# Performance work log

Measured on AMD Instinct MI355X. Metric: run time of the kernel, lower is better.

The kernel has to match this reference:

```python
import jax, jax.numpy as jnp
import numpy as np

N = 50000
E = 800000
IN_F = 128
HID = 128
OUT_F = 64
MU = 2.0
EPS = 1e-12


def setup_inputs() -> dict:
    key = jax.random.key(0)
    ks = jax.random.split(key, 20)
    d = {}
    d["x"] = jax.random.normal(ks[0], (N, IN_F), dtype=jnp.float32)
    d["edge_src"] = jax.random.randint(ks[1], (E,), 0, N, dtype=jnp.int32)
    d["edge_dst"] = jax.random.randint(ks[2], (E,), 0, N, dtype=jnp.int32)
    d["edge_val"] = jax.random.uniform(ks[3], (E,), dtype=jnp.float32)
    # layer 0: in=128 -> pool=128 -> out=128 (activation=relu)
    s0 = 1.0 / np.sqrt(IN_F)
    d["pool_w0"] = jax.random.uniform(ks[4], (IN_F, IN_F), jnp.float32, -s0, s0)
    d["pool_b0"] = jax.random.uniform(ks[5], (IN_F,), jnp.float32, -s0, s0)
    d["fc1_w0"] = jax.random.uniform(ks[6], (HID, IN_F), jnp.float32, -s0, s0)
    d["fc1_b0"] = jax.random.uniform(ks[7], (HID,), jnp.float32, -s0, s0)
    d["fc2_w0"] = jax.random.uniform(ks[8], (HID, IN_F), jnp.float32, -s0, s0)
    d["fc2_b0"] = jax.random.uniform(ks[9], (HID,), jnp.float32, -s0, s0)
    # layer 1 (final): in=128 -> pool=128 -> out=64 (no activation)
    s1 = 1.0 / np.sqrt(HID)
    d["pool_w1"] = jax.random.uniform(ks[10], (HID, HID), jnp.float32, -s1, s1)
    d["pool_b1"] = jax.random.uniform(ks[11], (HID,), jnp.float32, -s1, s1)
    d["fc1_w1"] = jax.random.uniform(ks[12], (OUT_F, HID), jnp.float32, -s1, s1)
    d["fc1_b1"] = jax.random.uniform(ks[13], (OUT_F,), jnp.float32, -s1, s1)
    d["fc2_w1"] = jax.random.uniform(ks[14], (OUT_F, HID), jnp.float32, -s1, s1)
    d["fc2_b1"] = jax.random.uniform(ks[15], (OUT_F,), jnp.float32, -s1, s1)
    return d


def _sage_conv(x, src, dst, val, pw, pb, w1, b1, w2, b2, act):
    # L2-normalize rows (F.normalize(x, dim=1))
    xn = x / jnp.maximum(jnp.linalg.norm(x, axis=1, keepdims=True), EPS)
    h = jax.nn.relu(xn @ pw.T + pb)               # [N, pool]
    h_mu = h ** MU                                # elementwise pow
    # spmm(adj, h_mu): gather source rows, scale by edge weight, scatter-add to dst rows
    agg = jax.ops.segment_sum(h_mu[src] * val[:, None], dst, num_segments=N)
    agg = agg ** (1.0 / MU)                       # generalized-mean root
    out = (h @ w1.T + b1) + (agg @ w2.T + b2)
    return jax.nn.relu(out) if act else out


def reference(x, edge_src, edge_dst, edge_val,
              pool_w0, pool_b0, fc1_w0, fc1_b0, fc2_w0, fc2_b0,
              pool_w1, pool_b1, fc1_w1, fc1_b1, fc2_w1, fc2_b1):
    h = _sage_conv(x, edge_src, edge_dst, edge_val,
                   pool_w0, pool_b0, fc1_w0, fc1_b0, fc2_w0, fc2_b0, act=True)
    out = _sage_conv(h, edge_src, edge_dst, edge_val,
                     pool_w1, pool_b1, fc1_w1, fc1_b1, fc2_w1, fc2_b1, act=False)
    return out
```

## Files before the change

### kernel.cpp

```cpp
#include <hip/hip_runtime.h>

#define FF 128
#define BCAP 8192
#define CHUNK 4096
#define PITCH 136
#define BSTRIDE 32
#define PBCACHE 6144

typedef __attribute__((ext_vector_type(8))) short short8;
typedef __attribute__((ext_vector_type(4))) float f32x4;
typedef __attribute__((ext_vector_type(4))) int i32x4;
typedef __attribute__((ext_vector_type(2))) int i32x2;

__device__ __forceinline__ unsigned short bf16_rne(float f) {
    unsigned u = __float_as_uint(f);
    u += 0x7fffu + ((u >> 16) & 1u);
    return (unsigned short)(u >> 16);
}
__device__ __forceinline__ float bf16_to_f32(unsigned short h) {
    return __uint_as_float(((unsigned)h) << 16);
}

__global__ __launch_bounds__(256, 2)
void poolpartA_kernel(const float* __restrict__ x,
                      const unsigned short* __restrict__ Wh, const unsigned short* __restrict__ Wl,
                      const float* __restrict__ bias,
                      unsigned short* __restrict__ hout,
                      const int* __restrict__ esrc, const int* __restrict__ edst,
                      const float* __restrict__ eval,
                      int* __restrict__ bucket_cnt, int2* __restrict__ ebuf,
                      int N, int E, int nchunks)
{
    __shared__ alignas(16) char smem[37888];
    const int t = threadIdx.x;

    if (blockIdx.x < nchunks) {
        int* cnt   = (int*)smem;
        int* sc    = cnt + 256;
        int* excl  = sc + 256;
        int* cur   = excl + 256;
        int* gbase = cur + 256;
        int2* staged = (int2*)(smem + 5 * 256 * 4);
        const int e0 = blockIdx.x * CHUNK;
        const int n  = min(CHUNK, E - e0);

        unsigned pk[16]; float vr[16];
        #pragma unroll
        for (int k = 0; k < 16; ++k) {
            const int i = t + k * 256;
            pk[k] = 0xFFFFFFFFu;
            if (i < n) {
                int d = edst[e0 + i];
                int s = esrc[e0 + i];
                pk[k] = (unsigned)((s & 0xffff) | (d << 16));
                vr[k] = eval[e0 + i];
            }
        }

        cnt[t] = 0;
        __syncthreads();
        #pragma unroll
        for (int k = 0; k < 16; ++k)
            if (pk[k] != 0xFFFFFFFFu) atomicAdd(&cnt[pk[k] >> 24], 1);
        __syncthreads();

        sc[t] = cnt[t];
        __syncthreads();
        #pragma unroll
        for (int off = 1; off < 256; off <<= 1) {
            int v = (t >= off) ? sc[t - off] : 0;
            __syncthreads();
            sc[t] += v;
            __syncthreads();
        }
        excl[t] = sc[t] - cnt[t];
        cur[t]  = excl[t];
        if (cnt[t] > 0) gbase[t] = atomicAdd(&bucket_cnt[t * BSTRIDE], cnt[t]);
        __syncthreads();

        #pragma unroll
        for (int k = 0; k < 16; ++k) {
            if (pk[k] != 0xFFFFFFFFu) {
                int b = pk[k] >> 24;
                int slot = atomicAdd(&cur[b], 1);
                staged[slot] = make_int2((int)pk[k], __float_as_int(vr[k]));
            }
        }
        __syncthreads();

        for (int p = t; p < n; p += 256) {
            int2 ent = staged[p];
            int b = ((unsigned)ent.x) >> 24;
            int gpos = gbase[b] + (p - excl[b]);
            ebuf[(size_t)b * BCAP + gpos] = ent;
        }
    } else {
        unsigned short* sX = (unsigned short*)smem;
        float* sNorm = (float*)(smem + 64 * PITCH * 2);
        const int tile = blockIdx.x - nchunks;

        #pragma unroll
        for (int rg = 0; rg < 2; ++rg) {
            const int row = rg * 32 + (t >> 3);
            const int c0  = (t & 7) * 16;
            const int n   = tile * 64 + row;
            const int base = row * PITCH + c0;
            float v[16];
            if (n < N) {
                const float4* p = (const float4*)(x + (size_t)n * FF + c0);
                #pragma unroll
                for (int i = 0; i < 4; ++i) {
                    float4 q = p[i];
                    v[4*i] = q.x; v[4*i+1] = q.y; v[4*i+2] = q.z; v[4*i+3] = q.w;
                }
            } else {
                #pragma unroll
                for (int i = 0; i < 16; ++i) v[i] = 0.f;
            }
            float ss = 0.f;
            #pragma unroll
            for (int i = 0; i < 16; ++i) ss = fmaf(v[i], v[i], ss);
            union { unsigned short u[8]; short8 s; } h0, h1;
            #pragma unroll
            for (int i = 0; i < 8; ++i) {
                h0.u[i] = bf16_rne(v[i]);
                h1.u[i] = bf16_rne(v[8 + i]);
            }
            *(short8*)&sX[base]     = h0.s;
            *(short8*)&sX[base + 8] = h1.s;
            ss += __shfl_xor(ss, 1);
            ss += __shfl_xor(ss, 2);
            ss += __shfl_xor(ss, 4);
            if ((t & 7) == 0) sNorm[row] = 1.0f / fmaxf(sqrtf(ss), 1e-12f);
        }
        __syncthreads();

        const int lane = t & 63, wave = t >> 6;
        const int quad = lane >> 4, l16 = lane & 15;

        short8 Bh[2][4], Bl[2][4];
        #pragma unroll
        for (int c = 0; c < 2; ++c) {
            const int jt = 2 * wave + c;
            #pragma unroll
            for (int tt = 0; tt < 4; ++tt) {
                const size_t o = ((size_t)(jt * 4 + tt) * 64 + lane) * 8;
                Bh[c][tt] = *(const short8*)&Wh[o];
                Bl[c][tt] = *(const short8*)&Wl[o];
            }
        }

        f32x4 acc[4][2];
        #pragma unroll
        for (int r = 0; r < 4; ++r)
            #pragma unroll
            for (int c = 0; c < 2; ++c) {
                f32x4 z = {0.f, 0.f, 0.f, 0.f};
                acc[r][c] = z;
            }

        #pragma unroll
        for (int tt = 0; tt < 4; ++tt) {
            short8 Ah[4];
            #pragma unroll
            for (int r = 0; r < 4; ++r)
                Ah[r] = *(const short8*)&sX[(r * 16 + l16) * PITCH + tt * 32 + quad * 8];
            #pragma unroll
            for (int c = 0; c < 2; ++c)
                #pragma unroll
                for (int r = 0; r < 4; ++r) {
                    acc[r][c] = __builtin_amdgcn_mfma_f32_16x16x32_bf16(Ah[r], Bh[c][tt], acc[r][c], 0, 0, 0);
                    acc[r][c] = __builtin_amdgcn_mfma_f32_16x16x32_bf16(Ah[r], Bl[c][tt], acc[r][c], 0, 0, 0);
                }
        }

        __syncthreads();
        #pragma unroll
        for (int c = 0; c < 2; ++c) {
            const int j = (2 * wave + c) * 16 + l16;
            const float bj = bias[j];
            #pragma unroll
            for (int r = 0; r < 4; ++r) {
                #pragma unroll
                for (int g = 0; g < 4; ++g) {
                    const int nl = r * 16 + quad * 4 + g;
                    float s = sNorm[nl];
                    float val = fmaf(acc[r][c][g], s, bj);
                    val = fmaxf(val, 0.f);
                    sX[nl * PITCH + j] = bf16_rne(val);
                }
            }
        }
        __syncthreads();
        #pragma unroll
        for (int rg = 0; rg < 2; ++rg) {
            const int row = rg * 32 + (t >> 3);
            const int c0  = (t & 7) * 16;
            const int n   = tile * 64 + row;
            if (n < N) {
                const int base = row * PITCH + c0;
                *(short8*)&hout[(size_t)n * FF + c0]     = *(short8*)&sX[base];
                *(short8*)&hout[(size_t)n * FF + c0 + 8] = *(short8*)&sX[base + 8];
            }
        }
    }
}

struct WPack {
    const float* src[6];
    unsigned short* hi[6];
    unsigned short* lo[6];
    int n[6];
};

__global__ __launch_bounds__(256)
void wprep_kernel(WPack p, int* __restrict__ bucket_cnt)
{
    if (blockIdx.x == 0) {
        for (int i = threadIdx.x; i < 256 * BSTRIDE; i += 256) bucket_cnt[i] = 0;
    }
    int id = blockIdx.x * 256 + threadIdx.x;
    #pragma unroll
    for (int i = 0; i < 6; ++i) {
        if (id < p.n[i]) {
            float f = p.src[i][id];
            unsigned short h = bf16_rne(f);
            const int j = id >> 7, k = id & 127;
            const int jt = j >> 4, l16 = j & 15;
            const int t = k >> 5, quad = (k >> 3) & 3, j8 = k & 7;
            const size_t o = ((size_t)((jt * 4 + t) * 4 + quad) * 16 + l16) * 8 + j8;
            p.hi[i][o] = h;
            p.lo[i][o] = bf16_rne(f - bf16_to_f32(h));
            return;
        }
        id -= p.n[i];
    }
}

__global__ __launch_bounds__(256)
void partB_kernel(const int* __restrict__ bucket_cnt, const int2* __restrict__ ebuf,
                  int* __restrict__ offsets, int2* __restrict__ edata,
                  int N, int E, int nbuck)
{
    __shared__ int pre[256], hist[256], sc[256], excl[256], cur[256];
    __shared__ int2 sBuf[PBCACHE];
    const int t = threadIdx.x;
    const int b = blockIdx.x;

    const int cnt_self = bucket_cnt[b * BSTRIDE];
    const int2* ib = ebuf + (size_t)b * BCAP;
    const bool useL = (cnt_self <= PBCACHE);

    if (useL)
        for (int i = t; i < cnt_self; i += 256) sBuf[i] = ib[i];

    pre[t] = (t < nbuck) ? bucket_cnt[t * BSTRIDE] : 0;
    hist[t] = 0;
    __syncthreads();
    #pragma unroll
    for (int off = 1; off < 256; off <<= 1) {
        int v = (t >= off) ? pre[t - off] : 0;
        __syncthreads();
        pre[t] += v;
        __syncthreads();
    }
    const int base = (b == 0) ? 0 : pre[b - 1];
    const int cnt  = cnt_self;

    for (int i = t; i < cnt; i += 256) {
        int2 ent = useL ? sBuf[i] : ib[i];
        atomicAdd(&hist[(((unsigned)ent.x) >> 16) & 255], 1);
    }
    __syncthreads();

    sc[t] = hist[t];
    __syncthreads();
    #pragma unroll
    for (int off = 1; off < 256; off <<= 1) {
        int v = (t >= off) ? sc[t - off] : 0;
        __syncthreads();
        sc[t] += v;
        __syncthreads();
    }
    excl[t] = sc[t] - hist[t];
    cur[t]  = excl[t];

    const int node = b * 256 + t;
    if (node <= N) offsets[node] = base + excl[t];
    __syncthreads();

    for (int i = t; i < cnt; i += 256) {
        int2 ent = useL ? sBuf[i] : ib[i];
        int l = (((unsigned)ent.x) >> 16) & 255;
        int pos = base + atomicAdd(&cur[l], 1);
        edata[pos] = make_int2(ent.x & 0xffff, ent.y);
    }
}

__device__ __forceinline__ void fma4sq(float4& a, float v, uint2 u) {
    float f0 = __uint_as_float(u.x << 16);
    float f1 = __uint_as_float(u.x & 0xffff0000u);
    float f2 = __uint_as_float(u.y << 16);
    float f3 = __uint_as_float(u.y & 0xffff0000u);
    a.x = fmaf(v * f0, f0, a.x);
    a.y = fmaf(v * f1, f1, a.y);
    a.z = fmaf(v * f2, f2, a.z);
    a.w = fmaf(v * f3, f3, a.w);
}

__device__ __forceinline__ i32x4 ldnt4(const int2* p) {
    return __builtin_nontemporal_load((const i32x4*)p);
}
__device__ __forceinline__ i32x2 ldnt2(const int2* p) {
    return __builtin_nontemporal_load((const i32x2*)p);
}

__global__ __launch_bounds__(256)
void agg_kernel(const unsigned short* __restrict__ hp, const int* __restrict__ offsets,
                const int2* __restrict__ edata,
                unsigned short* __restrict__ aggh, int N)
{
    const int w = blockIdx.x * 8 + (threadIdx.x >> 5);
    if (w >= N) return;
    const int l = threadIdx.x & 31;
    const size_t fo = (size_t)(l * 4);
    int e = offsets[w];
    const int end = offsets[w + 1];

    float4 a0 = {0,0,0,0}, a1 = {0,0,0,0}, a2 = {0,0,0,0}, a3 = {0,0,0,0};

    if ((e & 1) && e < end) {
        i32x2 ed = ldnt2(&edata[e]);
        uint2 u = *(const uint2*)&hp[(size_t)ed[0] * FF + fo];
        fma4sq(a0, __int_as_float(ed[1]), u);
        ++e;
    }
    for (; e + 7 < end; e += 8) {
        i32x4 p0 = ldnt4(&edata[e]);
        i32x4 p1 = ldnt4(&edata[e + 2]);
        i32x4 p2 = ldnt4(&edata[e + 4]);
        i32x4 p3 = ldnt4(&edata[e + 6]);
        uint2 u0 = *(const uint2*)&hp[(size_t)p0[0] * FF + fo];
        uint2 u1 = *(const uint2*)&hp[(size_t)p0[2] * FF + fo];
        uint2 u2 = *(const uint2*)&hp[(size_t)p1[0] * FF + fo];
        uint2 u3 = *(const uint2*)&hp[(size_t)p1[2] * FF + fo];
        uint2 u4 = *(const uint2*)&hp[(size_t)p2[0] * FF + fo];
        uint2 u5 = *(const uint2*)&hp[(size_t)p2[2] * FF + fo];
        uint2 u6 = *(const uint2*)&hp[(size_t)p3[0] * FF + fo];
        uint2 u7 = *(const uint2*)&hp[(size_t)p3[2] * FF + fo];
        fma4sq(a0, __int_as_float(p0[1]), u0);
        fma4sq(a1, __int_as_float(p0[3]), u1);
        fma4sq(a2, __int_as_float(p1[1]), u2);
        fma4sq(a3, __int_as_float(p1[3]), u3);
        fma4sq(a0, __int_as_float(p2[1]), u4);
        fma4sq(a1, __int_as_float(p2[3]), u5);
        fma4sq(a2, __int_as_float(p3[1]), u6);
        fma4sq(a3, __int_as_float(p3[3]), u7);
    }
    if (e + 3 < end) {
        i32x4 p0 = ldnt4(&edata[e]);
        i32x4 p1 = ldnt4(&edata[e + 2]);
        uint2 u0 = *(const uint2*)&hp[(size_t)p0[0] * FF + fo];
        uint2 u1 = *(const uint2*)&hp[(size_t)p0[2] * FF + fo];
        uint2 u2 = *(const uint2*)&hp[(size_t)p1[0] * FF + fo];
        uint2 u3 = *(const uint2*)&hp[(size_t)p1[2] * FF + fo];
        fma4sq(a0, __int_as_float(p0[1]), u0);
        fma4sq(a1, __int_as_float(p0[3]), u1);
        fma4sq(a2, __int_as_float(p1[1]), u2);
        fma4sq(a3, __int_as_float(p1[3]), u3);
        e += 4;
    }
    if (e + 1 < end) {
        i32x4 p = ldnt4(&edata[e]);
        uint2 u0 = *(const uint2*)&hp[(size_t)p[0] * FF + fo];
        uint2 u1 = *(const uint2*)&hp[(size_t)p[2] * FF + fo];
        fma4sq(a0, __int_as_float(p[1]), u0);
        fma4sq(a1, __int_as_float(p[3]), u1);
        e += 2;
    }
    if (e < end) {
        i32x2 ed = ldnt2(&edata[e]);
        uint2 u = *(const uint2*)&hp[(size_t)ed[0] * FF + fo];
        fma4sq(a0, __int_as_float(ed[1]), u);
    }

    float4 r;
    r.x = sqrtf(a0.x + a1.x + a2.x + a3.x);
    r.y = sqrtf(a0.y + a1.y + a2.y + a3.y);
    r.z = sqrtf(a0.z + a1.z + a2.z + a3.z);
    r.w = sqrtf(a0.w + a1.w + a2.w + a3.w);

    uint2 hv = { (unsigned)bf16_rne(r.x) | ((unsigned)bf16_rne(r.y) << 16),
                 (unsigned)bf16_rne(r.z) | ((unsigned)bf16_rne(r.w) << 16) };
    *(uint2*)&aggh[(size_t)w * FF + fo] = hv;
}

__global__ __launch_bounds__(256, 2)
void mm2pool_kernel(const unsigned short* __restrict__ hin,
                    const unsigned short* __restrict__ aggh,
                    const unsigned short* __restrict__ W1h, const unsigned short* __restrict__ W1l,
                    const unsigned short* __restrict__ W2h, const unsigned short* __restrict__ W2l,
                    const float* __restrict__ b1, const float* __restrict__ b2,
                    const unsigned short* __restrict__ PWh, const unsigned short* __restrict__ PWl,
                    const float* __restrict__ pb,
                    unsigned short* __restrict__ hout, int N)
{
    __shared__ unsigned short sH[64 * PITCH];
    __shared__ unsigned short sA[64 * PITCH];
    __shared__ float sNorm[64];

    const int tid  = threadIdx.x;
    const int tile = blockIdx.x;

    #pragma unroll
    for (int rg = 0; rg < 2; ++rg) {
        const int row = rg * 32 + (tid >> 3);
        const int c0  = (tid & 7) * 16;
        const int n   = tile * 64 + row;
        const int base = row * PITCH + c0;
        short8 z = {0,0,0,0,0,0,0,0};
        short8 a = z, b = z, c = z, d = z;
        if (n < N) {
            const short8* ph = (const short8*)(hin  + (size_t)n * FF + c0);
            const short8* pa = (const short8*)(aggh + (size_t)n * FF + c0);
            a = ph[0]; b = ph[1];
            c = pa[0]; d = pa[1];
        }
        *(short8*)&sH[base]     = a;
        *(short8*)&sH[base + 8] = b;
        *(short8*)&sA[base]     = c;
        *(short8*)&sA[base + 8] = d;
    }
    __syncthreads();

    const int lane = tid & 63, wave = tid >> 6;
    const int quad = lane >> 4, l16 = lane & 15;

    short8 B1hf[2][4], B1lf[2][4], B2hf[2][4], B2lf[2][4];
    #pragma unroll
    for (int c = 0; c < 2; ++c) {
        const int jt = 2 * wave + c;
        #pragma unroll
        for (int t = 0; t < 4; ++t) {
            const size_t o = ((size_t)(jt * 4 + t) * 64 + lane) * 8;
            B1hf[c][t] = *(const short8*)&W1h[o];
            B1lf[c][t] = *(const short8*)&W1l[o];
            B2hf[c][t] = *(const short8*)&W2h[o];
            B2lf[c][t] = *(const short8*)&W2l[o];
        }
    }

    f32x4 acc[4][2];
    #pragma unroll
    for (int r = 0; r < 4; ++r)
        #pragma unroll
        for (int c = 0; c < 2; ++c) {
            f32x4 z = {0.f, 0.f, 0.f, 0.f};
            acc[r][c] = z;
        }

    #pragma unroll
    for (int t = 0; t < 4; ++t) {
        short8 Hf[4], AH[4];
        #pragma unroll
        for (int r = 0; r < 4; ++r) {
            const int off = (r * 16 + l16) * PITCH + t * 32 + quad * 8;
            Hf[r] = *(const short8*)&sH[off];
            AH[r] = *(const short8*)&sA[off];
        }
        #pragma unroll
        for (int c = 0; c < 2; ++c)
            #pragma unroll
            for (int r = 0; r < 4; ++r) {
                acc[r][c] = __builtin_amdgcn_mfma_f32_16x16x32_bf16(Hf[r], B1hf[c][t], acc[r][c], 0, 0, 0);
                acc[r][c] = __builtin_amdgcn_mfma_f32_16x16x32_bf16(Hf[r], B1lf[c][t], acc[r][c], 0, 0, 0);
                acc[r][c] = __builtin_amdgcn_mfma_f32_16x16x32_bf16(AH[r], B2hf[c][t], acc[r][c], 0, 0, 0);
                acc[r][c] = __builtin_amdgcn_mfma_f32_16x16x32_bf16(AH[r], B2lf[c][t], acc[r][c], 0, 0, 0);
            }
    }

    __syncthreads();

    #pragma unroll
    for (int c = 0; c < 2; ++c) {
        const int j = (2 * wave + c) * 16 + l16;
        const float bj = b1[j] + b2[j];
        #pragma unroll
        for (int r = 0; r < 4; ++r) {
            #pragma unroll
            for (int g = 0; g < 4; ++g) {
                const int nl = r * 16 + quad * 4 + g;
                float val = fmaxf(acc[r][c][g] + bj, 0.f);
                sH[nl * PITCH + j] = bf16_rne(val);
            }
        }
    }
    __syncthreads();

    #pragma unroll
    for (int rg = 0; rg < 2; ++rg) {
        const int row = rg * 32 + (tid >> 3);
        const int c0  = (tid & 7) * 16;
        union { short8 s; unsigned short u[8]; } a, b;
        a.s = *(short8*)&sH[row * PITCH + c0];
        b.s = *(short8*)&sH[row * PITCH + c0 + 8];
        float ss = 0.f;
        #pragma unroll
        for (int i = 0; i < 8; ++i) {
            float fa = bf16_to_f32(a.u[i]);
            float fb = bf16_to_f32(b.u[i]);
            ss = fmaf(fa, fa, fmaf(fb, fb, ss));
        }
        ss += __shfl_xor(ss, 1);
        ss += __shfl_xor(ss, 2);
        ss += __shfl_xor(ss, 4);
        if ((tid & 7) == 0) sNorm[row] = 1.0f / fmaxf(sqrtf(ss), 1e-12f);
    }
    __syncthreads();

    short8 Ph[2][4], Pl[2][4];
    #pragma unroll
    for (int c = 0; c < 2; ++c) {
        const int jt = 2 * wave + c;
        #pragma unroll
        for (int t = 0; t < 4; ++t) {
            const size_t o = ((size_t)(jt * 4 + t) * 64 + lane) * 8;
            Ph[c][t] = *(const short8*)&PWh[o];
            Pl[c][t] = *(const short8*)&PWl[o];
        }
    }

    f32x4 acc2[4][2];
    #pragma unroll
    for (int r = 0; r < 4; ++r)
        #pragma unroll
        for (int c = 0; c < 2; ++c) {
            f32x4 z = {0.f, 0.f, 0.f, 0.f};
            acc2[r][c] = z;
        }

    #pragma unroll
    for (int t = 0; t < 4; ++t) {
        short8 Ah[4];
        #pragma unroll
        for (int r = 0; r < 4; ++r)
            Ah[r] = *(const short8*)&sH[(r * 16 + l16) * PITCH + t * 32 + quad * 8];
        #pragma unroll
        for (int c = 0; c < 2; ++c)
            #pragma unroll
            for (int r = 0; r < 4; ++r) {
                acc2[r][c] = __builtin_amdgcn_mfma_f32_16x16x32_bf16(Ah[r], Ph[c][t], acc2[r][c], 0, 0, 0);
                acc2[r][c] = __builtin_amdgcn_mfma_f32_16x16x32_bf16(Ah[r], Pl[c][t], acc2[r][c], 0, 0, 0);
            }
    }

    __syncthreads();
    #pragma unroll
    for (int c = 0; c < 2; ++c) {
        const int j = (2 * wave + c) * 16 + l16;
        const float pbj = pb[j];
        #pragma unroll
        for (int r = 0; r < 4; ++r) {
            #pragma unroll
            for (int g = 0; g < 4; ++g) {
                const int nl = r * 16 + quad * 4 + g;
                float s = sNorm[nl];
                float val = fmaxf(fmaf(acc2[r][c][g], s, pbj), 0.f);
                sA[nl * PITCH + j] = bf16_rne(val);
            }
        }
    }
    __syncthreads();
    #pragma unroll
    for (int rg = 0; rg < 2; ++rg) {
        const int row = rg * 32 + (tid >> 3);
        const int c0  = (tid & 7) * 16;
        const int n   = tile * 64 + row;
        if (n < N) {
            const int base = row * PITCH + c0;
            *(short8*)&hout[(size_t)n * FF + c0]     = *(short8*)&sA[base];
            *(short8*)&hout[(size_t)n * FF + c0 + 8] = *(short8*)&sA[base + 8];
        }
    }
}

#define OPITCH 68
__global__ __launch_bounds__(256, 2)
void mm2_final_kernel(const unsigned short* __restrict__ hin,
                      const unsigned short* __restrict__ aggh,
                      const unsigned short* __restrict__ W1h, const unsigned short* __restrict__ W1l,
                      const unsigned short* __restrict__ W2h, const unsigned short* __restrict__ W2l,
                      const float* __restrict__ b1, const float* __restrict__ b2,
                      float* __restrict__ out, int N)
{
    __shared__ unsigned short sH[64 * PITCH];
    __shared__ unsigned short sA[64 * PITCH];

    const int tid  = threadIdx.x;
    const int tile = blockIdx.x;

    #pragma unroll
    for (int rg = 0; rg < 2; ++rg) {
        const int row = rg * 32 + (tid >> 3);
        const int c0  = (tid & 7) * 16;
        const int n   = tile * 64 + row;
        const int base = row * PITCH + c0;
        short8 z = {0,0,0,0,0,0,0,0};
        short8 a = z, b = z, c = z, d = z;
        if (n < N) {
            const short8* ph = (const short8*)(hin  + (size_t)n * FF + c0);
            const short8* pa = (const short8*)(aggh + (size_t)n * FF + c0);
            a = ph[0]; b = ph[1];
            c = pa[0]; d = pa[1];
        }
        *(short8*)&sH[base]     = a;
        *(short8*)&sH[base + 8] = b;
        *(short8*)&sA[base]     = c;
        *(short8*)&sA[base + 8] = d;
    }
    __syncthreads();

    const int lane = tid & 63, wave = tid >> 6;
    const int quad = lane >> 4, l16 = lane & 15;

    short8 B1hf[4], B1lf[4], B2hf[4], B2lf[4];
    #pragma unroll
    for (int t = 0; t < 4; ++t) {
        const size_t o = ((size_t)(wave * 4 + t) * 64 + lane) * 8;
        B1hf[t] = *(const short8*)&W1h[o];
        B1lf[t] = *(const short8*)&W1l[o];
        B2hf[t] = *(const short8*)&W2h[o];
        B2lf[t] = *(const short8*)&W2l[o];
    }

    f32x4 acc[4];
    #pragma unroll
    for (int r = 0; r < 4; ++r) {
        f32x4 z = {0.f, 0.f, 0.f, 0.f};
        acc[r] = z;
    }

    #pragma unroll
    for (int t = 0; t < 4; ++t) {
        short8 Hf[4], AH[4];
        #pragma unroll
        for (int r = 0; r < 4; ++r) {
            const int off = (r * 16 + l16) * PITCH + t * 32 + quad * 8;
            Hf[r] = *(const short8*)&sH[off];
            AH[r] = *(const short8*)&sA[off];
        }
        #pragma unroll
        for (int r = 0; r < 4; ++r) {
            acc[r] = __builtin_amdgcn_mfma_f32_16x16x32_bf16(Hf[r], B1hf[t], acc[r], 0, 0, 0);
            acc[r] = __builtin_amdgcn_mfma_f32_16x16x32_bf16(Hf[r], B1lf[t], acc[r], 0, 0, 0);
            acc[r] = __builtin_amdgcn_mfma_f32_16x16x32_bf16(AH[r], B2hf[t], acc[r], 0, 0, 0);
            acc[r] = __builtin_amdgcn_mfma_f32_16x16x32_bf16(AH[r], B2lf[t], acc[r], 0, 0, 0);
        }
    }

    __syncthreads();
    float* sOut = (float*)sH;
    {
        const int j = wave * 16 + l16;
        const float bj = b1[j] + b2[j];
        #pragma unroll
        for (int r = 0; r < 4; ++r) {
            #pragma unroll
            for (int g = 0; g < 4; ++g) {
                const int nl = r * 16 + quad * 4 + g;
                sOut[nl * OPITCH + j] = acc[r][g] + bj;
            }
        }
    }
    __syncthreads();
    {
        const int row = tid >> 2;
        const int seg = tid & 3;
        const int n = tile * 64 + row;
        if (n < N) {
            const float4* src = (const float4*)&sOut[row * OPITCH + seg * 16];
            float4* dst = (float4*)&out[(size_t)n * 64 + seg * 16];
            #pragma unroll
            for (int i = 0; i < 4; ++i) dst[i] = src[i];
        }
    }
}

extern "C" void kernel_launch(void* const* d_in, const int* in_sizes, int n_in,
                              void* d_out, int out_size, void* d_ws, size_t ws_size,
                              hipStream_t stream) {
    const float* x    = (const float*)d_in[0];
    const int*   esrc = (const int*)d_in[1];
    const int*   edst = (const int*)d_in[2];
    const float* eval = (const float*)d_in[3];
    const float* pw0  = (const float*)d_in[4];
    const float* pb0  = (const float*)d_in[5];
    const float* f1w0 = (const float*)d_in[6];
    const float* f1b0 = (const float*)d_in[7];
    const float* f2w0 = (const float*)d_in[8];
    const float* f2b0 = (const float*)d_in[9];
    const float* pw1  = (const float*)d_in[10];
    const float* pb1  = (const float*)d_in[11];
    const float* f1w1 = (const float*)d_in[12];
    const float* f1b1 = (const float*)d_in[13];
    const float* f2w1 = (const float*)d_in[14];
    const float* f2b1 = (const float*)d_in[15];
    float* out = (float*)d_out;

    const int N = in_sizes[0] / FF;
    const int E = in_sizes[1];
    const int nbuck = (N + 255) / 256;

    char* ws = (char*)d_ws;
    const size_t planesz = (size_t)N * FF * 2;
    const size_t A = 256;
    size_t off = 0;
    unsigned short* h    = (unsigned short*)(ws + off); off += (planesz + A - 1) / A * A;
    unsigned short* h2   = (unsigned short*)(ws + off); off += (planesz + A - 1) / A * A;
    unsigned short* aggh = (unsigned short*)(ws + off); off += (planesz + A - 1) / A * A;
    int* offsets = (int*)(ws + off); off += ((size_t)(N + 1) * 4 + A - 1) / A * A;
    int* bucket_cnt = (int*)(ws + off); off += (size_t)256 * BSTRIDE * 4;
    int2* ebuf  = (int2*)(ws + off); off += (size_t)nbuck * BCAP * 8;
    int2* edata = (int2*)(ws + off); off += (size_t)E * 8;
    const int wsz[6] = {128 * FF, 128 * FF, 128 * FF, 128 * FF, 64 * FF, 64 * FF};
    unsigned short* whi[6];
    unsigned short* wlo[6];
    for (int i = 0; i < 6; ++i) {
        whi[i] = (unsigned short*)(ws + off); off += (size_t)wsz[i] * 2;
        wlo[i] = (unsigned short*)(ws + off); off += (size_t)wsz[i] * 2;
    }

    WPack pack;
    const float* wsrc[6] = {pw0, f1w0, f2w0, pw1, f1w1, f2w1};
    int wtotal = 0;
    for (int i = 0; i < 6; ++i) {
        pack.src[i] = wsrc[i]; pack.hi[i] = whi[i]; pack.lo[i] = wlo[i]; pack.n[i] = wsz[i];
        wtotal += wsz[i];
    }

    const int ntiles     = (N + 63) / 64;
    const int nodeblocks = (N + 7) / 8;
    const int nchunks    = (E + CHUNK - 1) / CHUNK;
    dim3 B(256);

    wprep_kernel<<<(wtotal + 255) / 256, B, 0, stream>>>(pack, bucket_cnt);

    poolpartA_kernel<<<nchunks + ntiles, B, 0, stream>>>(
        x, whi[0], wlo[0], pb0, h, esrc, edst, eval, bucket_cnt, ebuf, N, E, nchunks);

    partB_kernel<<<nbuck, B, 0, stream>>>(bucket_cnt, ebuf, offsets, edata, N, E, nbuck);

    agg_kernel<<<nodeblocks, B, 0, stream>>>(h, offsets, edata, aggh, N);

    mm2pool_kernel<<<ntiles, B, 0, stream>>>(
        h, aggh, whi[1], wlo[1], whi[2], wlo[2], f1b0, f2b0,
        whi[3], wlo[3], pb1, h2, N);

    agg_kernel<<<nodeblocks, B, 0, stream>>>(h2, offsets, edata, aggh, N);

    mm2_final_kernel<<<ntiles, B, 0, stream>>>(
        h2, aggh, whi[4], wlo[4], whi[5], wlo[5], f1b1, f2b1, out, N);
}
```

Baseline: 241.2 us.

## Split aggregation feature dimension across four blocks with 8 lanes per node

The sparse aggregation kernel previously gave each node a full 32-lane group covering all 128 features. Now each node's features are split into four 32-feature quarters handled by separate blocks, with 8 lanes per node and 32 nodes per block. The 8-edge unrolled loop is dropped in favour of a 4-edge loop. This packs more independent nodes into each wave to hide gather latency and uneven degree, but it reads edge data four times and issues narrower per-node gathers (64 bytes per row segment).

Result: slower. 284.3 us (+17.8%).

```diff
diff --git a/kernel.cpp b/kernel.cpp
--- a/kernel.cpp
+++ b/kernel.cpp
@@ -320,10 +320,11 @@
                 const int2* __restrict__ edata,
                 unsigned short* __restrict__ aggh, int N)
 {
-    const int w = blockIdx.x * 8 + (threadIdx.x >> 5);
+    const int q = blockIdx.x & 3;
+    const int w = (blockIdx.x >> 2) * 32 + (threadIdx.x >> 3);
     if (w >= N) return;
-    const int l = threadIdx.x & 31;
-    const size_t fo = (size_t)(l * 4);
+    const int l = threadIdx.x & 7;
+    const size_t fo = (size_t)(q * 32 + l * 4);
     int e = offsets[w];
     const int end = offsets[w + 1];
 
@@ -335,29 +336,7 @@
         fma4sq(a0, __int_as_float(ed[1]), u);
         ++e;
     }
-    for (; e + 7 < end; e += 8) {
-        i32x4 p0 = ldnt4(&edata[e]);
-        i32x4 p1 = ldnt4(&edata[e + 2]);
-        i32x4 p2 = ldnt4(&edata[e + 4]);
-        i32x4 p3 = ldnt4(&edata[e + 6]);
-        uint2 u0 = *(const uint2*)&hp[(size_t)p0[0] * FF + fo];
-        uint2 u1 = *(const uint2*)&hp[(size_t)p0[2] * FF + fo];
-        uint2 u2 = *(const uint2*)&hp[(size_t)p1[0] * FF + fo];
-        uint2 u3 = *(const uint2*)&hp[(size_t)p1[2] * FF + fo];
-        uint2 u4 = *(const uint2*)&hp[(size_t)p2[0] * FF + fo];
-        uint2 u5 = *(const uint2*)&hp[(size_t)p2[2] * FF + fo];
-        uint2 u6 = *(const uint2*)&hp[(size_t)p3[0] * FF + fo];
-        uint2 u7 = *(const uint2*)&hp[(size_t)p3[2] * FF + fo];
-        fma4sq(a0, __int_as_float(p0[1]), u0);
-        fma4sq(a1, __int_as_float(p0[3]), u1);
-        fma4sq(a2, __int_as_float(p1[1]), u2);
-        fma4sq(a3, __int_as_float(p1[3]), u3);
-        fma4sq(a0, __int_as_float(p2[1]), u4);
-        fma4sq(a1, __int_as_float(p2[3]), u5);
-        fma4sq(a2, __int_as_float(p3[1]), u6);
-        fma4sq(a3, __int_as_float(p3[3]), u7);
-    }
-    if (e + 3 < end) {
+    for (; e + 3 < end; e += 4) {
         i32x4 p0 = ldnt4(&edata[e]);
         i32x4 p1 = ldnt4(&edata[e + 2]);
         uint2 u0 = *(const uint2*)&hp[(size_t)p0[0] * FF + fo];
@@ -368,7 +347,6 @@
         fma4sq(a1, __int_as_float(p0[3]), u1);
         fma4sq(a2, __int_as_float(p1[1]), u2);
         fma4sq(a3, __int_as_float(p1[3]), u3);
-        e += 4;
     }
     if (e + 1 < end) {
         i32x4 p = ldnt4(&edata[e]);
@@ -739,7 +717,7 @@
     }
 
     const int ntiles     = (N + 63) / 64;
-    const int nodeblocks = (N + 7) / 8;
+    const int nodeblocks = ((N + 31) / 32) * 4;
     const int nchunks    = (E + CHUNK - 1) / CHUNK;
     dim3 B(256);
 
```
